# Kernel optimization log

Hardware: AMD Instinct MI355X
Metric: run time of the kernel (lower is better)

## Reference

```python
import jax, jax.numpy as jnp
import numpy as np
from jax import lax

B, HCH, NCODES, H, W = 16, 32, 256, 256, 256

def conv2d(x, w, b, pad):
    y = lax.conv_general_dilated(x, w, (1, 1), [(pad, pad), (pad, pad)],
                                 dimension_numbers=('NCHW', 'OIHW', 'NCHW'))
    return y + b[None, :, None, None]

def vq(z, codebook):
    # z: (B,C,H,W); codebook: (K,C)
    zf = jnp.transpose(z, (0, 2, 3, 1)).reshape(-1, z.shape[1])  # (BHW,C)
    dists = (zf ** 2).sum(1, keepdims=True) + (codebook ** 2).sum(1) - 2.0 * zf @ codebook.T
    idx = jnp.argmin(dists, axis=1)
    zq = codebook[idx].reshape(z.shape[0], z.shape[2], z.shape[3], z.shape[1])
    zq = jnp.transpose(zq, (0, 3, 1, 2))
    # straight-through estimator
    return z + lax.stop_gradient(zq - z)

def setup_inputs() -> dict:
    key = jax.random.key(0)
    ks = jax.random.split(key, 12)
    s = lambda k, shp, scale=0.1: (jax.random.normal(k, shp, jnp.float32) * scale)
    return {
        'x': jax.random.normal(ks[0], (B, 1, H, W), jnp.float32),
        'stem_w': s(ks[1], (HCH, 1, 3, 3)),
        'stem_b': s(ks[2], (HCH,)),
        'up1_w': s(ks[3], (HCH, HCH, 3, 3)),
        'up1_b': s(ks[4], (HCH,)),
        'up2_w': s(ks[5], (HCH, HCH, 1, 1)),
        'up2_b': s(ks[6], (HCH,)),
        'tau_w': s(ks[7], (HCH, HCH, 1, 1)),
        'tau_b': s(ks[8], (HCH,)),
        'codebook': jax.random.uniform(ks[9], (NCODES, HCH), jnp.float32,
                                       -1.0 / NCODES, 1.0 / NCODES),
        'dec_w': s(ks[10], (1, HCH, 1, 1)),
        'dec_b': s(ks[11], (1,)),
        'n_steps': 5,
    }

def reference(x, stem_w, stem_b, up1_w, up1_b, up2_w, up2_b, tau_w, tau_b,
              codebook, dec_w, dec_b, n_steps):
    state = jax.nn.relu(conv2d(x, stem_w, stem_b, 1))
    for t in range(n_steps):
        delta = conv2d(jax.nn.relu(conv2d(state, up1_w, up1_b, 1)), up2_w, up2_b, 0)
        beta = jax.nn.sigmoid(conv2d(state, tau_w, tau_b, 0))
        state = beta * state + (1.0 - beta) * delta
        state = vq(state, codebook)  # vq_every = 1
    return jax.nn.sigmoid(conv2d(state, dec_w, dec_b, 0))
```

## Files before the change

### kernel.cpp

```cpp
#include <hip/hip_runtime.h>
#include <hip/hip_bf16.h>

#define BATCH 16
#define HH 256
#define WW 256
#define NPIX (BATCH*HH*WW)
#define NSTEPS 5
#define CBS 40

#define W1F 0
#define W2F 9216
#define WTF 10240
#define CBF 11264
#define IDF 19456
#define W1P 20480
#define W2P 29696
#define WTP 30720
#define IDP 31744
#define CBP 32768
#define FRAGS_TOT 40960

using u16 = unsigned short;
using u32 = unsigned int;
using u8  = unsigned char;

typedef __attribute__((ext_vector_type(8))) short bf8_t;
typedef __attribute__((ext_vector_type(4))) float f4_t;

#define MFMA16 __builtin_amdgcn_mfma_f32_16x16x32_bf16

#define DPPMIN(v, CTRL) do { \
    u32 _o = (u32)__builtin_amdgcn_update_dpp((int)(v), (int)(v), (CTRL), 0xF, 0xF, false); \
    (v) = _o < (v) ? _o : (v); } while (0)

#define LDS_ORDER() asm volatile("" ::: "memory")

__device__ __forceinline__ float bf2f(u32 u) {
    union { u32 i; float f; } v; v.i = u << 16; return v.f;
}
__device__ __forceinline__ u16 f2bf(float f) {
    union { float f; u32 i; } v; v.f = f;
    u32 x = v.i;
    x += 0x7fffu + ((x >> 16) & 1u);
    return (u16)(x >> 16);
}
__device__ __forceinline__ u32 pack2bf(float a, float b) {
    __hip_bfloat162 h2 = __float22bfloat162_rn(float2{a, b});
    union { __hip_bfloat162 h; u32 u; } v; v.h = h2; return v.u;
}
__device__ __forceinline__ float ldin(const void* p, int i, int f32) {
    return f32 ? ((const float*)p)[i] : bf2f(((const u16*)p)[i]);
}
__device__ __forceinline__ u16 ldbf(const void* p, int i, int f32) {
    return f32 ? f2bf(((const float*)p)[i]) : ((const u16*)p)[i];
}
__device__ __forceinline__ int sniff_f32(const void* xraw) {
    const u32* xw = (const u32*)xraw;
    int cnt = 0;
    for (int j = 0; j < 64; j++) {
        u32 w = xw[j];
        float flo = bf2f(w & 0xffffu);
        float a = fabsf(flo);
        if (flo == 0.0f || (a >= 6e-8f && a <= 64.0f)) cnt++;
    }
    return (cnt < 32) ? 1 : 0;
}
__device__ __forceinline__ int chperm(int kp) { return (kp >> 1) | ((kp & 1) << 4); }

__global__ void prep_kernel(const void* x,
    const void* stem_w, const void* stem_b, const void* up1_w, const void* up1_b,
    const void* up2_w, const void* up2_b, const void* tau_w, const void* tau_b,
    const void* cb, const void* dec_w, const void* dec_b,
    u16* frags, u16* cb_bf,
    float* cn2, float* cadj, float* decdot, float* wf0,
    float* up1_bf, float* up2_bf, float* tau_bf, float* stem_bf, int* flag)
{
    int f32 = sniff_f32(x);
    int i = blockIdx.x * 256 + threadIdx.x;
    if (i == 0) *flag = f32;
    if (i < 9216) {
        int slot = i >> 9, rem = i & 511, lane = rem >> 3, j = rem & 7;
        int tap = slot >> 1, nt = slot & 1;
        int co = nt*16 + (lane & 15), ci = (lane >> 4)*8 + j;
        frags[W1F + i] = ldbf(up1_w, (co*32+ci)*9 + tap, f32);
        return;
    }
    i -= 9216;
    if (i < 1024) {
        int nt = i >> 9, rem = i & 511, lane = rem >> 3, j = rem & 7;
        int co = nt*16 + (lane & 15), k = (lane >> 4)*8 + j;
        frags[W2F + i] = ldbf(up2_w, co*32 + k, f32);
        return;
    }
    i -= 1024;
    if (i < 1024) {
        int nt = i >> 9, rem = i & 511, lane = rem >> 3, j = rem & 7;
        int co = nt*16 + (lane & 15), k = (lane >> 4)*8 + j;
        frags[WTF + i] = ldbf(tau_w, co*32 + k, f32);
        return;
    }
    i -= 1024;
    if (i < 8192) {
        int nt = i >> 9, rem = i & 511, lane = rem >> 3, j = rem & 7;
        int code = nt*16 + (lane & 15), c = (lane >> 4)*8 + j;
        frags[CBF + i] = ldbf(cb, code*32 + c, f32);
        return;
    }
    i -= 8192;
    if (i < 1024) {
        int s = i >> 9, rem = i & 511, lane = rem >> 3, j = rem & 7;
        int colq = lane & 15, quad = lane >> 4;
        frags[IDF + i] = ((quad*8 + j) == (colq + s*16)) ? (u16)0x3F80 : (u16)0;
        return;
    }
    i -= 1024;
    if (i < 9216) {
        int slot = i >> 9, rem = i & 511, lane = rem >> 3, j = rem & 7;
        int tap = slot >> 1, nt = slot & 1;
        int co = nt*16 + (lane & 15), ci = chperm((lane >> 4)*8 + j);
        frags[W1P + i] = ldbf(up1_w, (co*32+ci)*9 + tap, f32);
        return;
    }
    i -= 9216;
    if (i < 1024) {
        int nt = i >> 9, rem = i & 511, lane = rem >> 3, j = rem & 7;
        int co = nt*16 + (lane & 15), k = chperm((lane >> 4)*8 + j);
        frags[W2P + i] = ldbf(up2_w, co*32 + k, f32);
        return;
    }
    i -= 1024;
    if (i < 1024) {
        int nt = i >> 9, rem = i & 511, lane = rem >> 3, j = rem & 7;
        int co = nt*16 + (lane & 15), k = chperm((lane >> 4)*8 + j);
        frags[WTP + i] = ldbf(tau_w, co*32 + k, f32);
        return;
    }
    i -= 1024;
    if (i < 1024) {
        int s = i >> 9, rem = i & 511, lane = rem >> 3, j = rem & 7;
        int colq = lane & 15, quad = lane >> 4;
        int ch = chperm(quad*8 + j);
        frags[IDP + i] = (ch == (colq + s*16)) ? (u16)0x3F80 : (u16)0;
        return;
    }
    i -= 1024;
    if (i < 8192) {
        int nt = i >> 9, rem = i & 511, lane = rem >> 3, j = rem & 7;
        int code = nt*16 + (lane & 15), c = chperm((lane >> 4)*8 + j);
        frags[CBP + i] = ldbf(cb, code*32 + c, f32);
        return;
    }
    i -= 8192;
    if (i < 257*CBS) {
        int row = i / CBS, p = i - row*CBS;
        cb_bf[i] = (p < 32 && row < 256) ? ldbf(cb, row*32 + chperm(p), f32) : (u16)0;
        return;
    }
    i -= 257*CBS;
    if (i < 256) {
        float s = 0.f;
        for (int c = 0; c < 32; c++) { float v = ldin(cb, i*32+c, f32); s += v*v; }
        cn2[i] = 0.5f * s;
        return;
    }
    i -= 256;
    if (i < 256) {
        float s = 0.f;
        for (int c = 0; c < 32; c++) { float v = ldin(cb, i*32+c, f32); s += v*v; }
        cadj[i] = 0.25f * (0.5f * s) + 0.5f;
        return;
    }
    i -= 256;
    if (i < 256) {
        float s = ldin(dec_b, 0, f32);
        for (int c = 0; c < 32; c++) s += ldin(dec_w, c, f32) * ldin(cb, i*32+c, f32);
        decdot[i] = s;
        return;
    }
    i -= 256;
    if (i < 288) {
        int tap = i >> 5, co = i & 31;
        wf0[i] = ldin(stem_w, co*9 + tap, f32);
        return;
    }
    i -= 288;
    if (i < 32) { up1_bf[i]  = ldin(up1_b, i, f32); return; }
    i -= 32;
    if (i < 32) { up2_bf[i]  = ldin(up2_b, i, f32); return; }
    i -= 32;
    if (i < 32) { tau_bf[i]  = ldin(tau_b, i, f32); return; }
    i -= 32;
    if (i < 32) { stem_bf[i] = ldin(stem_b, i, f32); return; }
}

__global__ __launch_bounds__(256) void step0_kernel(
    const void* __restrict__ xraw, const int* __restrict__ flagp,
    u8* __restrict__ idx_out,
    const u16* __restrict__ fragsg, const float* __restrict__ cn2,
    const float* __restrict__ up1_b, const float* __restrict__ up2_b,
    const float* __restrict__ tau_b, const float* __restrict__ wf0,
    const float* __restrict__ stem_bf)
{
    __shared__ __align__(16) u16 smem[31872];
    u16* w1f   = smem;
    u16* w2f   = smem + 9216;
    u16* wtf   = smem + 10240;
    u16* cbf   = smem + 11264;
    u16* tileq = smem + 19456;
    u16* hzb   = smem + 29824;
    float* xs  = (float*)hzb;

    int tid = threadIdx.x;
    int lane = tid & 63, wave = tid >> 6;
    int col = lane & 15, quad = lane >> 4;
    int b = blockIdx.z, x0 = blockIdx.x * 16, y0 = blockIdx.y * 16;

    bf8_t id0 = *(const bf8_t*)&fragsg[IDP + (0*64+lane)*8];
    bf8_t id1 = *(const bf8_t*)&fragsg[IDP + (1*64+lane)*8];

    {
        const uint4* s4 = (const uint4*)(fragsg + W1P);
        uint4* d4 = (uint4*)smem;
        for (int i = tid; i < 1408; i += 256) d4[i] = s4[i];
        const uint4* c4 = (const uint4*)(fragsg + CBP);
        uint4* e4 = (uint4*)cbf;
        for (int i = tid; i < 1024; i += 256) e4[i] = c4[i];
    }

    {
        int f32 = *flagp;
        for (int pp = tid; pp < 400; pp += 256) {
            int r = pp / 20, c = pp - r*20;
            int gy = y0 - 2 + r, gx = x0 - 2 + c;
            float v = 0.f;
            if ((unsigned)gy < 256u && (unsigned)gx < 256u)
                v = ldin(xraw, (b << 16) | (gy << 8) | gx, f32);
            xs[pp] = v;
        }
        __syncthreads();
        for (int pp = tid; pp < 324; pp += 256) {
            int r = pp / 18, c = pp - r*18;
            int gy = y0 - 1 + r, gx = x0 - 1 + c;
            uint4 qv[4] = {{0,0,0,0},{0,0,0,0},{0,0,0,0},{0,0,0,0}};
            if ((unsigned)gy < 256u && (unsigned)gx < 256u) {
                float acc[32];
#pragma unroll
                for (int co = 0; co < 32; co++) acc[co] = stem_bf[co];
#pragma unroll
                for (int tap = 0; tap < 9; tap++) {
                    float v = xs[(r + tap/3)*20 + (c + tap%3)];
                    const float* w = &wf0[tap*32];
#pragma unroll
                    for (int co = 0; co < 32; co++) acc[co] = fmaf(v, w[co], acc[co]);
                }
                u32* ow = (u32*)qv;
#pragma unroll
                for (int m = 0; m < 16; m++)
                    ow[m] = pack2bf(fmaxf(acc[m], 0.f), fmaxf(acc[m+16], 0.f));
            }
#pragma unroll
            for (int q = 0; q < 4; q++)
                *(uint4*)&tileq[(q*324 + pp)*8] = qv[q];
        }
    }
    __syncthreads();

    float cn2adj[16];
#pragma unroll
    for (int nt = 0; nt < 16; nt++) cn2adj[nt] = 0.25f*cn2[nt*16+col] + 0.5f;
    float bu1C0 = up1_b[col], bu1C1 = up1_b[col+16];
    float bu2_0 = up2_b[col], bu2_1 = up2_b[col+16];
    float bt0 = tau_b[col],   bt1 = tau_b[col+16];
    u16* hzw = &hzb[wave*512];
    u32* hz32 = (u32*)hzw;
    int wy = wave * 4;
    f4_t kz = {0.f,0.f,0.f,0.f};

    bf8_t rows[4][3];
#pragma unroll
    for (int i = 0; i < 4; i++)
#pragma unroll
        for (int dx = 0; dx < 3; dx++)
            rows[i][dx] = *(const bf8_t*)&tileq[(quad*324 + (wy+i)*18 + col+dx)*8];

#pragma unroll
    for (int rrp = 0; rrp < 2; rrp++) {
        if (rrp) {
#pragma unroll
            for (int dx = 0; dx < 3; dx++) {
                rows[0][dx] = rows[2][dx];
                rows[1][dx] = rows[3][dx];
                rows[2][dx] = *(const bf8_t*)&tileq[(quad*324 + (wy+4)*18 + col+dx)*8];
                rows[3][dx] = *(const bf8_t*)&tileq[(quad*324 + (wy+5)*18 + col+dx)*8];
            }
        }
        f4_t aA0 = kz, aA1 = kz, aB0 = kz, aB1 = kz;
#pragma unroll
        for (int t = 0; t < 9; t++) {
            int dy = t/3, dx = t - dy*3;
            bf8_t wA = *(const bf8_t*)&w1f[((t*2+0)*64 + lane)*8];
            bf8_t wB = *(const bf8_t*)&w1f[((t*2+1)*64 + lane)*8];
            aA0 = MFMA16(rows[dy  ][dx], wA, aA0, 0, 0, 0);
            aA1 = MFMA16(rows[dy  ][dx], wB, aA1, 0, 0, 0);
            aB0 = MFMA16(rows[dy+1][dx], wA, aB0, 0, 0, 0);
            aB1 = MFMA16(rows[dy+1][dx], wB, aB1, 0, 0, 0);
        }
#pragma unroll
        for (int r = 0; r < 4; r++) {
            int px = quad*4 + r;
            hz32[px*16 + col] = pack2bf(fmaxf(aA0[r] + bu1C0, 0.f),
                                        fmaxf(aA1[r] + bu1C1, 0.f));
        }
        LDS_ORDER();
        bf8_t hA0 = *(const bf8_t*)&hzw[col*32 + quad*8];
        LDS_ORDER();
#pragma unroll
        for (int r = 0; r < 4; r++) {
            int px = quad*4 + r;
            hz32[px*16 + col] = pack2bf(fmaxf(aB0[r] + bu1C0, 0.f),
                                        fmaxf(aB1[r] + bu1C1, 0.f));
        }
        LDS_ORDER();
        bf8_t hA1 = *(const bf8_t*)&hzw[col*32 + quad*8];
        LDS_ORDER();

        bf8_t w20 = *(const bf8_t*)&w2f[(0*64+lane)*8];
        bf8_t w21 = *(const bf8_t*)&w2f[(1*64+lane)*8];
        bf8_t wt0 = *(const bf8_t*)&wtf[(0*64+lane)*8];
        bf8_t wt1 = *(const bf8_t*)&wtf[(1*64+lane)*8];
        bf8_t sA0 = rows[1][1], sA1 = rows[2][1];
        f4_t d00 = MFMA16(hA0, w20, kz, 0, 0, 0);
        f4_t d01 = MFMA16(hA0, w21, kz, 0, 0, 0);
        f4_t d10 = MFMA16(hA1, w20, kz, 0, 0, 0);
        f4_t d11 = MFMA16(hA1, w21, kz, 0, 0, 0);
        f4_t t00 = MFMA16(sA0, wt0, kz, 0, 0, 0);
        f4_t t01 = MFMA16(sA0, wt1, kz, 0, 0, 0);
        f4_t t10 = MFMA16(sA1, wt0, kz, 0, 0, 0);
        f4_t t11 = MFMA16(sA1, wt1, kz, 0, 0, 0);
        f4_t S0l = MFMA16(sA0, id0, kz, 0, 0, 0);
        f4_t S0h = MFMA16(sA0, id1, kz, 0, 0, 0);
        f4_t S1l = MFMA16(sA1, id0, kz, 0, 0, 0);
        f4_t S1h = MFMA16(sA1, id1, kz, 0, 0, 0);

#pragma unroll
        for (int r = 0; r < 4; r++) {
            int px = quad*4 + r;
            float dl0 = d00[r] + bu2_0, tv0 = t00[r] + bt0;
            float be0 = 1.0f / (1.0f + __expf(-tv0));
            float dl1 = d01[r] + bu2_1, tv1 = t01[r] + bt1;
            float be1 = 1.0f / (1.0f + __expf(-tv1));
            hz32[px*16 + col] = pack2bf(-0.25f * (dl0 + be0*(S0l[r] - dl0)),
                                        -0.25f * (dl1 + be1*(S0h[r] - dl1)));
        }
        LDS_ORDER();
        bf8_t zA0 = *(const bf8_t*)&hzw[col*32 + quad*8];
        LDS_ORDER();
#pragma unroll
        for (int r = 0; r < 4; r++) {
            int px = quad*4 + r;
            float dl0 = d10[r] + bu2_0, tv0 = t10[r] + bt0;
            float be0 = 1.0f / (1.0f + __expf(-tv0));
            float dl1 = d11[r] + bu2_1, tv1 = t11[r] + bt1;
            float be1 = 1.0f / (1.0f + __expf(-tv1));
            hz32[px*16 + col] = pack2bf(-0.25f * (dl0 + be0*(S1l[r] - dl0)),
                                        -0.25f * (dl1 + be1*(S1h[r] - dl1)));
        }
        LDS_ORDER();
        bf8_t zA1 = *(const bf8_t*)&hzw[col*32 + quad*8];
        LDS_ORDER();

        u32 b0[4], b1[4];
#pragma unroll
        for (int r = 0; r < 4; r++) { b0[r] = 0xFFFFFFFFu; b1[r] = 0xFFFFFFFFu; }
#pragma unroll
        for (int nt = 0; nt < 16; nt++) {
            bf8_t cf = *(const bf8_t*)&cbf[(nt*64 + lane)*8];
            f4_t ci = {cn2adj[nt], cn2adj[nt], cn2adj[nt], cn2adj[nt]};
            f4_t s0 = MFMA16(zA0, cf, ci, 0, 0, 0);
            f4_t s1 = MFMA16(zA1, cf, ci, 0, 0, 0);
            u32 code = (u32)(nt*16) | (u32)col;
#pragma unroll
            for (int r = 0; r < 4; r++) {
                u32 k0 = (__builtin_bit_cast(u32, s0[r]) & 0xFFFFFF00u) | code;
                u32 k1 = (__builtin_bit_cast(u32, s1[r]) & 0xFFFFFF00u) | code;
                b0[r] = k0 < b0[r] ? k0 : b0[r];
                b1[r] = k1 < b1[r] ? k1 : b1[r];
            }
        }
#pragma unroll
        for (int r = 0; r < 4; r++) {
            DPPMIN(b0[r], 0x121); DPPMIN(b0[r], 0x122);
            DPPMIN(b0[r], 0x124); DPPMIN(b0[r], 0x128);
            DPPMIN(b1[r], 0x121); DPPMIN(b1[r], 0x122);
            DPPMIN(b1[r], 0x124); DPPMIN(b1[r], 0x128);
        }
        int yr = y0 + wy + rrp*2;
        if (col < 4) {
            idx_out[(b*256 + yr    )*256 + x0 + quad*4 + col] = (u8)(b0[col] & 255u);
            idx_out[(b*256 + yr + 1)*256 + x0 + quad*4 + col] = (u8)(b1[col] & 255u);
        }
    }
}

__global__ __launch_bounds__(256) void step1_kernel(
    const u8* __restrict__ idx_in, u8* __restrict__ idx_out,
    const u16* __restrict__ fragsg, const u16* __restrict__ cbr_g,
    const float* __restrict__ cadj_g,
    const float* __restrict__ up1_b, const float* __restrict__ up2_b,
    const float* __restrict__ tau_b)
{
    __shared__ __align__(16) u16 smem[24104];
    u16* w1f = smem;
    u16* w2f = smem + 9216;
    u16* wtf = smem + 10240;
    u16* cbr = smem + 11264;
    float* cadjf = (float*)(smem + 21544);
    u16* hzb = smem + 22056;

    int tid = threadIdx.x;
    int lane = tid & 63, wave = tid >> 6;
    int col = lane & 15, quad = lane >> 4;
    int b = blockIdx.z, x0 = blockIdx.x * 16, y0 = blockIdx.y * 32;
    int wy = wave * 4;

    bf8_t id0 = *(const bf8_t*)&fragsg[IDP + (0*64+lane)*8];
    bf8_t id1 = *(const bf8_t*)&fragsg[IDP + (1*64+lane)*8];

    {
        const uint4* s4 = (const uint4*)(fragsg + W1P);
        uint4* d4 = (uint4*)smem;
        for (int i = tid; i < 1408; i += 256) d4[i] = s4[i];
        const uint4* c4 = (const uint4*)cbr_g;
        uint4* e4 = (uint4*)cbr;
        for (int i = tid; i < 1285; i += 256) e4[i] = c4[i];
        const uint4* a4 = (const uint4*)cadj_g;
        uint4* f4p = (uint4*)cadjf;
        if (tid < 64) f4p[tid] = a4[tid];
    }
    __syncthreads();

    float bu1C0 = up1_b[col], bu1C1 = up1_b[col+16];
    float bu2_0 = up2_b[col], bu2_1 = up2_b[col+16];
    float bt0 = tau_b[col],   bt1 = tau_b[col+16];
    u16* hzw = &hzb[wave*512];
    u32* hz32 = (u32*)hzw;
    f4_t kz = {0.f,0.f,0.f,0.f};

    for (int th = 0; th < 2; th++) {
        int yb = y0 + th*16;

        u32 kp[6];
#pragma unroll
        for (int tr = 0; tr < 6; tr++) {
            u32 pk = 0;
#pragma unroll
            for (int dx = 0; dx < 3; dx++) {
                int gy = yb - 1 + wy + tr, gx = x0 - 1 + col + dx;
                bool ok = ((unsigned)gy < 256u) & ((unsigned)gx < 256u);
                u32 c = ok ? (u32)idx_in[(b << 16) | (gy << 8) | gx] : 256u;
                pk |= c << (9*dx);
            }
            kp[tr] = pk;
        }

        f4_t acc[4][2];
#pragma unroll
        for (int r4 = 0; r4 < 4; r4++) { acc[r4][0] = kz; acc[r4][1] = kz; }
        bf8_t sA[4];
#pragma unroll
        for (int t = 0; t < 9; t++) {
            int dy = t/3, dx = t - dy*3;
            bf8_t wA = *(const bf8_t*)&w1f[((t*2+0)*64 + lane)*8];
            bf8_t wB = *(const bf8_t*)&w1f[((t*2+1)*64 + lane)*8];
#pragma unroll
            for (int r4 = 0; r4 < 4; r4++) {
                int k = (int)((kp[r4+dy] >> (9*dx)) & 511u);
                bf8_t f = *(const bf8_t*)&cbr[k*CBS + quad*8];
                if (t == 4) sA[r4] = f;
                acc[r4][0] = MFMA16(f, wA, acc[r4][0], 0, 0, 0);
                acc[r4][1] = MFMA16(f, wB, acc[r4][1], 0, 0, 0);
            }
        }

        bf8_t w20 = *(const bf8_t*)&w2f[(0*64+lane)*8];
        bf8_t w21 = *(const bf8_t*)&w2f[(1*64+lane)*8];
        bf8_t wt0 = *(const bf8_t*)&wtf[(0*64+lane)*8];
        bf8_t wt1 = *(const bf8_t*)&wtf[(1*64+lane)*8];

        bf8_t zA[4];
#pragma unroll
        for (int r4 = 0; r4 < 4; r4++) {
#pragma unroll
            for (int r = 0; r < 4; r++) {
                int px = quad*4 + r;
                hz32[px*16 + col] = pack2bf(fmaxf(acc[r4][0][r] + bu1C0, 0.f),
                                            fmaxf(acc[r4][1][r] + bu1C1, 0.f));
            }
            LDS_ORDER();
            bf8_t hA = *(const bf8_t*)&hzw[col*32 + quad*8];
            LDS_ORDER();
            f4_t d0 = MFMA16(hA, w20, kz, 0, 0, 0);
            f4_t d1 = MFMA16(hA, w21, kz, 0, 0, 0);
            f4_t t0 = MFMA16(sA[r4], wt0, kz, 0, 0, 0);
            f4_t t1 = MFMA16(sA[r4], wt1, kz, 0, 0, 0);
            f4_t Sl = MFMA16(sA[r4], id0, kz, 0, 0, 0);
            f4_t Sh = MFMA16(sA[r4], id1, kz, 0, 0, 0);
#pragma unroll
            for (int r = 0; r < 4; r++) {
                int px = quad*4 + r;
                float dl0 = d0[r] + bu2_0, tv0 = t0[r] + bt0;
                float be0 = 1.0f / (1.0f + __expf(-tv0));
                float dl1 = d1[r] + bu2_1, tv1 = t1[r] + bt1;
                float be1 = 1.0f / (1.0f + __expf(-tv1));
                hz32[px*16 + col] = pack2bf(-0.25f * (dl0 + be0*(Sl[r] - dl0)),
                                            -0.25f * (dl1 + be1*(Sh[r] - dl1)));
            }
            LDS_ORDER();
            zA[r4] = *(const bf8_t*)&hzw[col*32 + quad*8];
            LDS_ORDER();
        }

        u32 bk[4][4];
#pragma unroll
        for (int r4 = 0; r4 < 4; r4++)
#pragma unroll
            for (int r = 0; r < 4; r++) bk[r4][r] = 0xFFFFFFFFu;
#pragma unroll
        for (int nt = 0; nt < 16; nt++) {
            bf8_t cf = *(const bf8_t*)&cbr[(nt*16 + col)*CBS + quad*8];
            float ca = cadjf[nt*16 + col];
            f4_t ci = {ca, ca, ca, ca};
            u32 code = (u32)(nt*16) | (u32)col;
#pragma unroll
            for (int r4 = 0; r4 < 4; r4++) {
                f4_t sc = MFMA16(zA[r4], cf, ci, 0, 0, 0);
#pragma unroll
                for (int r = 0; r < 4; r++) {
                    u32 k0 = (__builtin_bit_cast(u32, sc[r]) & 0xFFFFFF00u) | code;
                    bk[r4][r] = k0 < bk[r4][r] ? k0 : bk[r4][r];
                }
            }
        }
#pragma unroll
        for (int r4 = 0; r4 < 4; r4++) {
#pragma unroll
            for (int r = 0; r < 4; r++) {
                DPPMIN(bk[r4][r], 0x121); DPPMIN(bk[r4][r], 0x122);
                DPPMIN(bk[r4][r], 0x124); DPPMIN(bk[r4][r], 0x128);
            }
            int yr = yb + wy + r4;
            if (col < 4)
                idx_out[(b*256 + yr)*256 + x0 + quad*4 + col] = (u8)(bk[r4][col] & 255u);
        }
    }
}

__global__ __launch_bounds__(256) void dec_kernel(const u8* __restrict__ idx,
        const float* __restrict__ decdot, const int* __restrict__ flagp,
        void* __restrict__ out)
{
    int p = blockIdx.x * 256 + threadIdx.x;
    float s = decdot[idx[p]];
    float r = 1.0f / (1.0f + __expf(-s));
    if (*flagp) ((float*)out)[p] = r;
    else        ((u16*)out)[p]   = f2bf(r);
}

extern "C" void kernel_launch(void* const* d_in, const int* in_sizes, int n_in,
                              void* d_out, int out_size, void* d_ws, size_t ws_size,
                              hipStream_t stream)
{
    const void* x      = d_in[0];
    const void* stem_w = d_in[1];
    const void* stem_b = d_in[2];
    const void* up1_w  = d_in[3];
    const void* up1_b  = d_in[4];
    const void* up2_w  = d_in[5];
    const void* up2_b  = d_in[6];
    const void* tau_w  = d_in[7];
    const void* tau_b  = d_in[8];
    const void* cb     = d_in[9];
    const void* dec_w  = d_in[10];
    const void* dec_b  = d_in[11];

    char* ws = (char*)d_ws;
    size_t off = 0;
    auto carve = [&](size_t bytes) -> void* {
        void* p = ws + off;
        off += (bytes + 255) & ~(size_t)255;
        return p;
    };
    u8*    idxA    = (u8*)   carve(NPIX);
    u8*    idxB    = (u8*)   carve(NPIX);
    u16*   frags   = (u16*)  carve(FRAGS_TOT * 2);
    u16*   cb_bf   = (u16*)  carve(257*CBS * 2);
    float* cn2     = (float*)carve(256 * 4);
    float* cadj    = (float*)carve(256 * 4);
    float* decdot  = (float*)carve(256 * 4);
    float* wf0     = (float*)carve(288 * 4);
    float* up1_bf  = (float*)carve(32 * 4);
    float* up2_bf  = (float*)carve(32 * 4);
    float* tau_bf  = (float*)carve(32 * 4);
    float* stem_bf = (float*)carve(32 * 4);
    int*   flag    = (int*)  carve(4);

    prep_kernel<<<205, 256, 0, stream>>>(x, stem_w, stem_b, up1_w, up1_b,
        up2_w, up2_b, tau_w, tau_b, cb, dec_w, dec_b,
        frags, cb_bf, cn2, cadj, decdot, wf0,
        up1_bf, up2_bf, tau_bf, stem_bf, flag);

    dim3 g0(WW/16, HH/16, BATCH);
    step0_kernel<<<g0, 256, 0, stream>>>(x, flag, idxA,
        frags, cn2, up1_bf, up2_bf, tau_bf, wf0, stem_bf);
    dim3 g1(WW/16, HH/32, BATCH);
    u8* cur = idxA; u8* nxt = idxB;
    for (int t = 1; t < NSTEPS; t++) {
        step1_kernel<<<g1, 256, 0, stream>>>(cur, nxt, frags, cb_bf, cadj,
                                             up1_bf, up2_bf, tau_bf);
        u8* tmp = cur; cur = nxt; nxt = tmp;
    }
    dec_kernel<<<NPIX/256, 256, 0, stream>>>(cur, decdot, flag, d_out);
}
```

Measured before the change: 454.9 us.

## Read weights from global memory and fold -0.25 scale into weights for occupancy

Stops staging conv weight fragments (and in step0 the codebook fragments) in shared memory; they are now read directly from global/L2 per wave, shrinking LDS so more blocks fit per CU, with launch bounds requesting 4 blocks. The -0.25 distance scale is folded into up2 weights, up2 bias and the identity fragment so the blend no longer multiplies per element. The trade is repeated global loads of the weights in the inner MFMA loop instead of LDS reads.

```diff
diff --git a/kernel.cpp b/kernel.cpp
--- a/kernel.cpp
+++ b/kernel.cpp
@@ -125,7 +125,7 @@
     if (i < 1024) {
         int nt = i >> 9, rem = i & 511, lane = rem >> 3, j = rem & 7;
         int co = nt*16 + (lane & 15), k = chperm((lane >> 4)*8 + j);
-        frags[W2P + i] = ldbf(up2_w, co*32 + k, f32);
+        frags[W2P + i] = f2bf(-0.25f * ldin(up2_w, co*32 + k, f32));
         return;
     }
     i -= 1024;
@@ -140,7 +140,7 @@
         int s = i >> 9, rem = i & 511, lane = rem >> 3, j = rem & 7;
         int colq = lane & 15, quad = lane >> 4;
         int ch = chperm(quad*8 + j);
-        frags[IDP + i] = (ch == (colq + s*16)) ? (u16)0x3F80 : (u16)0;
+        frags[IDP + i] = (ch == (colq + s*16)) ? (u16)0xBE80 : (u16)0;
         return;
     }
     i -= 1024;
@@ -186,14 +186,14 @@
     i -= 288;
     if (i < 32) { up1_bf[i]  = ldin(up1_b, i, f32); return; }
     i -= 32;
-    if (i < 32) { up2_bf[i]  = ldin(up2_b, i, f32); return; }
+    if (i < 32) { up2_bf[i]  = -0.25f * ldin(up2_b, i, f32); return; }
     i -= 32;
     if (i < 32) { tau_bf[i]  = ldin(tau_b, i, f32); return; }
     i -= 32;
     if (i < 32) { stem_bf[i] = ldin(stem_b, i, f32); return; }
 }
 
-__global__ __launch_bounds__(256) void step0_kernel(
+__global__ __launch_bounds__(256, 4) void step0_kernel(
     const void* __restrict__ xraw, const int* __restrict__ flagp,
     u8* __restrict__ idx_out,
     const u16* __restrict__ fragsg, const float* __restrict__ cn2,
@@ -201,14 +201,15 @@
     const float* __restrict__ tau_b, const float* __restrict__ wf0,
     const float* __restrict__ stem_bf)
 {
-    __shared__ __align__(16) u16 smem[31872];
-    u16* w1f   = smem;
-    u16* w2f   = smem + 9216;
-    u16* wtf   = smem + 10240;
-    u16* cbf   = smem + 11264;
-    u16* tileq = smem + 19456;
-    u16* hzb   = smem + 29824;
+    __shared__ __align__(16) u16 smem[12416];
+    u16* tileq = smem;
+    u16* hzb   = smem + 10368;
     float* xs  = (float*)hzb;
+
+    const u16* __restrict__ w1g = fragsg + W1P;
+    const u16* __restrict__ w2g = fragsg + W2P;
+    const u16* __restrict__ wtg = fragsg + WTP;
+    const u16* __restrict__ cbg = fragsg + CBP;
 
     int tid = threadIdx.x;
     int lane = tid & 63, wave = tid >> 6;
@@ -217,15 +218,6 @@
 
     bf8_t id0 = *(const bf8_t*)&fragsg[IDP + (0*64+lane)*8];
     bf8_t id1 = *(const bf8_t*)&fragsg[IDP + (1*64+lane)*8];
-
-    {
-        const uint4* s4 = (const uint4*)(fragsg + W1P);
-        uint4* d4 = (uint4*)smem;
-        for (int i = tid; i < 1408; i += 256) d4[i] = s4[i];
-        const uint4* c4 = (const uint4*)(fragsg + CBP);
-        uint4* e4 = (uint4*)cbf;
-        for (int i = tid; i < 1024; i += 256) e4[i] = c4[i];
-    }
 
     {
         int f32 = *flagp;
@@ -298,8 +290,8 @@
 #pragma unroll
         for (int t = 0; t < 9; t++) {
             int dy = t/3, dx = t - dy*3;
-            bf8_t wA = *(const bf8_t*)&w1f[((t*2+0)*64 + lane)*8];
-            bf8_t wB = *(const bf8_t*)&w1f[((t*2+1)*64 + lane)*8];
+            bf8_t wA = *(const bf8_t*)&w1g[((t*2+0)*64 + lane)*8];
+            bf8_t wB = *(const bf8_t*)&w1g[((t*2+1)*64 + lane)*8];
             aA0 = MFMA16(rows[dy  ][dx], wA, aA0, 0, 0, 0);
             aA1 = MFMA16(rows[dy  ][dx], wB, aA1, 0, 0, 0);
             aB0 = MFMA16(rows[dy+1][dx], wA, aB0, 0, 0, 0);
@@ -324,10 +316,10 @@
         bf8_t hA1 = *(const bf8_t*)&hzw[col*32 + quad*8];
         LDS_ORDER();
 
-        bf8_t w20 = *(const bf8_t*)&w2f[(0*64+lane)*8];
-        bf8_t w21 = *(const bf8_t*)&w2f[(1*64+lane)*8];
-        bf8_t wt0 = *(const bf8_t*)&wtf[(0*64+lane)*8];
-        bf8_t wt1 = *(const bf8_t*)&wtf[(1*64+lane)*8];
+        bf8_t w20 = *(const bf8_t*)&w2g[(0*64+lane)*8];
+        bf8_t w21 = *(const bf8_t*)&w2g[(1*64+lane)*8];
+        bf8_t wt0 = *(const bf8_t*)&wtg[(0*64+lane)*8];
+        bf8_t wt1 = *(const bf8_t*)&wtg[(1*64+lane)*8];
         bf8_t sA0 = rows[1][1], sA1 = rows[2][1];
         f4_t d00 = MFMA16(hA0, w20, kz, 0, 0, 0);
         f4_t d01 = MFMA16(hA0, w21, kz, 0, 0, 0);
@@ -349,8 +341,8 @@
             float be0 = 1.0f / (1.0f + __expf(-tv0));
             float dl1 = d01[r] + bu2_1, tv1 = t01[r] + bt1;
             float be1 = 1.0f / (1.0f + __expf(-tv1));
-            hz32[px*16 + col] = pack2bf(-0.25f * (dl0 + be0*(S0l[r] - dl0)),
-                                        -0.25f * (dl1 + be1*(S0h[r] - dl1)));
+            hz32[px*16 + col] = pack2bf(dl0 + be0*(S0l[r] - dl0),
+                                        dl1 + be1*(S0h[r] - dl1));
         }
         LDS_ORDER();
         bf8_t zA0 = *(const bf8_t*)&hzw[col*32 + quad*8];
@@ -362,8 +354,8 @@
             float be0 = 1.0f / (1.0f + __expf(-tv0));
             float dl1 = d11[r] + bu2_1, tv1 = t11[r] + bt1;
             float be1 = 1.0f / (1.0f + __expf(-tv1));
-            hz32[px*16 + col] = pack2bf(-0.25f * (dl0 + be0*(S1l[r] - dl0)),
-                                        -0.25f * (dl1 + be1*(S1h[r] - dl1)));
+            hz32[px*16 + col] = pack2bf(dl0 + be0*(S1l[r] - dl0),
+                                        dl1 + be1*(S1h[r] - dl1));
         }
         LDS_ORDER();
         bf8_t zA1 = *(const bf8_t*)&hzw[col*32 + quad*8];
@@ -374,7 +366,7 @@
         for (int r = 0; r < 4; r++) { b0[r] = 0xFFFFFFFFu; b1[r] = 0xFFFFFFFFu; }
 #pragma unroll
         for (int nt = 0; nt < 16; nt++) {
-            bf8_t cf = *(const bf8_t*)&cbf[(nt*64 + lane)*8];
+            bf8_t cf = *(const bf8_t*)&cbg[(nt*64 + lane)*8];
             f4_t ci = {cn2adj[nt], cn2adj[nt], cn2adj[nt], cn2adj[nt]};
             f4_t s0 = MFMA16(zA0, cf, ci, 0, 0, 0);
             f4_t s1 = MFMA16(zA1, cf, ci, 0, 0, 0);
@@ -402,20 +394,21 @@
     }
 }
 
-__global__ __launch_bounds__(256) void step1_kernel(
+__global__ __launch_bounds__(256, 4) void step1_kernel(
     const u8* __restrict__ idx_in, u8* __restrict__ idx_out,
     const u16* __restrict__ fragsg, const u16* __restrict__ cbr_g,
     const float* __restrict__ cadj_g,
     const float* __restrict__ up1_b, const float* __restrict__ up2_b,
     const float* __restrict__ tau_b)
 {
-    __shared__ __align__(16) u16 smem[24104];
-    u16* w1f = smem;
-    u16* w2f = smem + 9216;
-    u16* wtf = smem + 10240;
-    u16* cbr = smem + 11264;
-    float* cadjf = (float*)(smem + 21544);
-    u16* hzb = smem + 22056;
+    __shared__ __align__(16) u16 smem[14888];
+    u16* cbr = smem;
+    u16* w2f = smem + 10280;
+    u16* wtf = smem + 11304;
+    float* cadjf = (float*)(smem + 12328);
+    u16* hzb = smem + 12840;
+
+    const u16* __restrict__ w1g = fragsg + W1P;
 
     int tid = threadIdx.x;
     int lane = tid & 63, wave = tid >> 6;
@@ -427,9 +420,9 @@
     bf8_t id1 = *(const bf8_t*)&fragsg[IDP + (1*64+lane)*8];
 
     {
-        const uint4* s4 = (const uint4*)(fragsg + W1P);
-        uint4* d4 = (uint4*)smem;
-        for (int i = tid; i < 1408; i += 256) d4[i] = s4[i];
+        const uint4* s4 = (const uint4*)(fragsg + W2P);
+        uint4* d4 = (uint4*)w2f;
+        for (int i = tid; i < 256; i += 256) d4[i] = s4[i];
         const uint4* c4 = (const uint4*)cbr_g;
         uint4* e4 = (uint4*)cbr;
         for (int i = tid; i < 1285; i += 256) e4[i] = c4[i];
@@ -470,8 +463,8 @@
 #pragma unroll
         for (int t = 0; t < 9; t++) {
             int dy = t/3, dx = t - dy*3;
-            bf8_t wA = *(const bf8_t*)&w1f[((t*2+0)*64 + lane)*8];
-            bf8_t wB = *(const bf8_t*)&w1f[((t*2+1)*64 + lane)*8];
+            bf8_t wA = *(const bf8_t*)&w1g[((t*2+0)*64 + lane)*8];
+            bf8_t wB = *(const bf8_t*)&w1g[((t*2+1)*64 + lane)*8];
 #pragma unroll
             for (int r4 = 0; r4 < 4; r4++) {
                 int k = (int)((kp[r4+dy] >> (9*dx)) & 511u);
@@ -512,8 +505,8 @@
                 float be0 = 1.0f / (1.0f + __expf(-tv0));
                 float dl1 = d1[r] + bu2_1, tv1 = t1[r] + bt1;
                 float be1 = 1.0f / (1.0f + __expf(-tv1));
-                hz32[px*16 + col] = pack2bf(-0.25f * (dl0 + be0*(Sl[r] - dl0)),
-                                            -0.25f * (dl1 + be1*(Sh[r] - dl1)));
+                hz32[px*16 + col] = pack2bf(dl0 + be0*(Sl[r] - dl0),
+                                            dl1 + be1*(Sh[r] - dl1));
             }
             LDS_ORDER();
             zA[r4] = *(const bf8_t*)&hzw[col*32 + quad*8];
```

Result: slower. 677.1 us (+48.8%).
